# Performance work log

Hardware: AMD Instinct MI355X
Metric: run time of the kernel (lower is better)

Reference implementation:

```python
import jax, jax.numpy as jnp
import numpy as np

B, N, C, H = 8, 1024, 768, 12
D = C // H  # 64


def setup_inputs() -> dict:
    key = jax.random.key(0)
    ks = jax.random.split(key, 6)
    x = jax.random.normal(ks[0], (B, N, C), dtype=jnp.float32)
    pad_mask = jnp.ones((B, N), dtype=jnp.int32)
    # params (torch Linear stored transposed; here kept as (in, out) for x @ W)
    s = 1.0 / np.sqrt(C)
    w_attn = jax.random.uniform(ks[1], (C, 3 * C), jnp.float32, -s, s)
    b_attn = jax.random.uniform(ks[2], (3 * C,), jnp.float32, -s, s)
    w_proj = jax.random.uniform(ks[3], (C, C), jnp.float32, -s, s)
    b_proj = jax.random.uniform(ks[4], (C,), jnp.float32, -s, s)
    return {"x": x, "pad_mask": pad_mask, "w_attn": w_attn,
            "b_attn": b_attn, "w_proj": w_proj, "b_proj": b_proj}


def reference(x, pad_mask, w_attn, b_attn, w_proj, b_proj):
    # qkv projection
    qkv = x @ w_attn + b_attn                      # [B,N,3C]
    q, k, v = jnp.split(qkv, 3, axis=-1)
    q = q.reshape(B, N, H, D).transpose(0, 2, 1, 3)  # [B,H,N,D]
    k = k.reshape(B, N, H, D).transpose(0, 2, 1, 3)
    v = v.reshape(B, N, H, D).transpose(0, 2, 1, 3)
    scale = 1.0 / np.sqrt(D)
    att = jnp.einsum('bhqd,bhkd->bhqk', q, k) * scale  # [B,H,N,N]
    # NOTE: original code's causal masked_fill is non-in-place and discarded,
    # so the causal mask is NOT applied. Only the pad mask (over query rows) is.
    pm = pad_mask.reshape(B, 1, N, 1)
    att = jnp.where(pm == 0, -jnp.inf, att)
    att = jax.nn.softmax(att, axis=-1)
    out = jnp.einsum('bhqk,bhkd->bhqd', att, v)     # [B,H,N,D]
    out = out.transpose(0, 2, 1, 3).reshape(B, N, C)
    # dropout layers are identity in eval mode
    return out @ w_proj + b_proj
```

## Files before the change

### kernel.cpp

```cpp
#include <hip/hip_runtime.h>
#include <hip/hip_bf16.h>

#define B_  8
#define N_  1024
#define C_  768
#define H_  12
#define D_  64
#define C3  2304
#define C2  1536

typedef unsigned short ushort_t;
typedef __attribute__((ext_vector_type(8))) short bf16x8;
typedef __attribute__((ext_vector_type(4))) float f32x4;
typedef __attribute__((ext_vector_type(4))) unsigned int u32x4;
typedef __attribute__((ext_vector_type(2))) unsigned int u32x2;

__device__ __forceinline__ ushort_t f2bf(float f) {
    union { float f; unsigned int i; } v;
    v.f = f;
    unsigned int x = v.i;
    if ((x & 0x7f800000u) == 0x7f800000u && (x & 0x007fffffu))
        return (ushort_t)((x >> 16) | 0x0040u);
    return (ushort_t)((x + 0x7fffu + ((x >> 16) & 1u)) >> 16);
}

__device__ __forceinline__ void st1(float* p, float v) { *p = v; }
__device__ __forceinline__ void st1(ushort_t* p, float v) { *p = f2bf(v); }

__global__ __launch_bounds__(256) void cvt_bf16(
    const float* __restrict__ X, ushort_t* __restrict__ Y, int n)
{
    int i = (blockIdx.x * 256 + threadIdx.x) * 4;
    if (i < n) {
        float4 f = *reinterpret_cast<const float4*>(X + i);
        ushort4 o;
        o.x = f2bf(f.x); o.y = f2bf(f.y); o.z = f2bf(f.z); o.w = f2bf(f.w);
        *reinterpret_cast<ushort4*>(Y + i) = o;
    }
}

__global__ __launch_bounds__(256) void transpose_to_bf16(
    const float* __restrict__ W, ushort_t* __restrict__ WT, int K, int Nn)
{
    __shared__ float t[32][33];
    const int n0 = blockIdx.x * 32, k0 = blockIdx.y * 32;
    const int tx = threadIdx.x & 31, ty = threadIdx.x >> 5;
    #pragma unroll
    for (int i = 0; i < 4; ++i) {
        const int k = ty + i * 8;
        t[k][tx] = W[(size_t)(k0 + k) * Nn + n0 + tx];
    }
    __syncthreads();
    #pragma unroll
    for (int i = 0; i < 4; ++i) {
        const int n = ty + i * 8;
        WT[(size_t)(n0 + n) * K + k0 + tx] = f2bf(t[tx][n]);
    }
}

#define GBK 64

__device__ __forceinline__ void gld_lds16(const ushort_t* g, ushort_t* lds) {
    __builtin_amdgcn_global_load_lds(
        (const __attribute__((address_space(1))) void*)g,
        (__attribute__((address_space(3))) void*)lds, 16, 0, 0);
}

template<typename TO, bool SCALEQ>
__global__ __launch_bounds__(256) void gemm_mfma(
    const ushort_t* __restrict__ A, const ushort_t* __restrict__ BT,
    const float* __restrict__ bias, TO* __restrict__ Y, int ldY,
    ushort_t* __restrict__ vtOut, int M, int K, int Nn)
{
    __shared__ ushort_t As[128 * GBK];
    __shared__ ushort_t Bs[128 * GBK];

    const int tid  = threadIdx.x;
    const int wave = tid >> 6;
    const int lane = tid & 63;
    const int row0 = blockIdx.y * 128;
    const int col0 = blockIdx.x * 128;
    const int wr   = (wave >> 1) * 64;
    const int wc   = (wave & 1) * 64;
    const int l15  = lane & 15;
    const int quad = lane >> 4;
    const int l7   = l15 & 7;

    const int srow = lane >> 3;
    const int sg   = (lane & 7) ^ srow;

    f32x4 acc[4][4] = {};

    for (int k0 = 0; k0 < K; k0 += GBK) {
        __syncthreads();
        #pragma unroll
        for (int it = 0; it < 4; ++it) {
            const int baseRow = wave * 32 + it * 8;
            const int r = baseRow + srow;
            gld_lds16(&A [(size_t)(row0 + r) * K + k0 + sg * 8], &As[baseRow * GBK]);
            gld_lds16(&BT[(size_t)(col0 + r) * K + k0 + sg * 8], &Bs[baseRow * GBK]);
        }
        __syncthreads();

        #pragma unroll
        for (int kc = 0; kc < 2; ++kc) {
            bf16x8 af[4], bf[4];
            #pragma unroll
            for (int i = 0; i < 4; ++i) {
                const int aslot = (kc * 4 + quad) ^ l7;
                af[i] = *reinterpret_cast<const bf16x8*>(
                    &As[(wr + i * 16 + l15) * GBK + aslot * 8]);
                bf[i] = *reinterpret_cast<const bf16x8*>(
                    &Bs[(wc + i * 16 + l15) * GBK + aslot * 8]);
            }
            #pragma unroll
            for (int i = 0; i < 4; ++i)
                #pragma unroll
                for (int j = 0; j < 4; ++j)
                    acc[i][j] = __builtin_amdgcn_mfma_f32_16x16x32_bf16(
                        af[i], bf[j], acc[i][j], 0, 0, 0);
        }
    }

    const float qs = (SCALEQ && (col0 + wc) < C_) ? 0.1803368801f : 1.0f;

    if (vtOut != nullptr && col0 >= C2) {
        #pragma unroll
        for (int i = 0; i < 4; ++i) {
            const int r0 = row0 + wr + i * 16 + quad * 4;
            const int bb = r0 >> 10;
            const int n  = r0 & 1023;
            #pragma unroll
            for (int j = 0; j < 4; ++j) {
                const int c  = col0 + wc + j * 16 + l15;
                const int cv = c - C2;
                const int hh = cv >> 6, d = cv & 63;
                const float bv = bias[c];
                ushort4 o;
                o.x = f2bf(acc[i][j][0] + bv);
                o.y = f2bf(acc[i][j][1] + bv);
                o.z = f2bf(acc[i][j][2] + bv);
                o.w = f2bf(acc[i][j][3] + bv);
                *reinterpret_cast<ushort4*>(
                    &vtOut[((size_t)(bb * H_ + hh) * D_ + d) * N_ + n]) = o;
            }
        }
    } else {
        #pragma unroll
        for (int i = 0; i < 4; ++i) {
            const int r = row0 + wr + i * 16 + quad * 4;
            #pragma unroll
            for (int j = 0; j < 4; ++j) {
                const int c = col0 + wc + j * 16 + l15;
                const float bv = bias[c];
                #pragma unroll
                for (int t = 0; t < 4; ++t)
                    st1(&Y[(size_t)(r + t) * ldY + c], (acc[i][j][t] + bv) * qs);
            }
        }
    }
}

__global__ __launch_bounds__(256) void attn_mfma(
    const ushort_t* __restrict__ qk, const ushort_t* __restrict__ vt,
    const int* __restrict__ pad_mask, ushort_t* __restrict__ y)
{
    __shared__ __align__(16) ushort_t KV[2 * 64 * 64];
    ushort_t* const Ks  = KV;
    ushort_t* const Vts = KV + 64 * 64;

    const int tid  = threadIdx.x;
    const int wave = tid >> 6;
    const int lane = tid & 63;
    const int l15  = lane & 15;
    const int quad = lane >> 4;
    const int l7   = l15 & 7;

    const int qt = blockIdx.x & 7;
    const int h  = (blockIdx.x >> 3) % H_;
    const int b  = blockIdx.x / (8 * H_);
    const int q0 = qt * 128 + wave * 32;

    const ushort_t* qkB = qk + (size_t)b * N_ * C2;
    const ushort_t* vtB = vt + ((size_t)(b * H_ + h)) * D_ * N_;
    const int ho = h * D_;

    bf16x8 qf[2][2];
    #pragma unroll
    for (int rt = 0; rt < 2; ++rt)
        #pragma unroll
        for (int kc = 0; kc < 2; ++kc)
            qf[rt][kc] = *reinterpret_cast<const bf16x8*>(
                &qkB[(size_t)(q0 + rt * 16 + l15) * C2 + ho + kc * 32 + quad * 8]);

    int mrow[2][4];
    #pragma unroll
    for (int rt = 0; rt < 2; ++rt)
        #pragma unroll
        for (int t = 0; t < 4; ++t)
            mrow[rt][t] = pad_mask[b * N_ + q0 + rt * 16 + quad * 4 + t];

    f32x4 oacc[2][4] = {};
    float den[2] = {};

    const int srow = lane >> 3;
    const int sg   = (lane & 7) ^ srow;

    for (int k0 = 0; k0 < N_; k0 += 64) {
        __syncthreads();
        #pragma unroll
        for (int it = 0; it < 2; ++it) {
            const int base = wave * 16 + it * 8;
            const int r = base + srow;
            gld_lds16(&qkB[(size_t)(k0 + r) * C2 + C_ + ho + sg * 8],
                      &Ks[base * 64]);
            gld_lds16(&vtB[(size_t)r * N_ + k0 + sg * 8],
                      &Vts[base * 64]);
        }
        __syncthreads();

        f32x4 s[2][4] = {};
        #pragma unroll
        for (int kc = 0; kc < 2; ++kc) {
            bf16x8 kf[4];
            #pragma unroll
            for (int ct = 0; ct < 4; ++ct) {
                const int slot = (kc * 4 + quad) ^ l7;
                kf[ct] = *reinterpret_cast<const bf16x8*>(
                    &Ks[(ct * 16 + l15) * 64 + slot * 8]);
            }
            __builtin_amdgcn_s_setprio(1);
            #pragma unroll
            for (int rt = 0; rt < 2; ++rt)
                #pragma unroll
                for (int ct = 0; ct < 4; ++ct)
                    s[rt][ct] = __builtin_amdgcn_mfma_f32_16x16x32_bf16(
                        kf[ct], qf[rt][kc], s[rt][ct], 0, 0, 0);
            __builtin_amdgcn_s_setprio(0);
        }

        unsigned pk[2][4][2];
        #pragma unroll
        for (int rt = 0; rt < 2; ++rt)
            #pragma unroll
            for (int ct = 0; ct < 4; ++ct) {
                const unsigned x0 = __float_as_uint(
                    __builtin_amdgcn_exp2f(s[rt][ct][0])) + 0x8000u;
                const unsigned x1 = __float_as_uint(
                    __builtin_amdgcn_exp2f(s[rt][ct][1])) + 0x8000u;
                const unsigned x2 = __float_as_uint(
                    __builtin_amdgcn_exp2f(s[rt][ct][2])) + 0x8000u;
                const unsigned x3 = __float_as_uint(
                    __builtin_amdgcn_exp2f(s[rt][ct][3])) + 0x8000u;
                const unsigned c0 = (x0 >> 16) | (x1 & 0xffff0000u);
                const unsigned c1 = (x2 >> 16) | (x3 & 0xffff0000u);
                den[rt] += __uint_as_float(c0 << 16)
                         + __uint_as_float(c0 & 0xffff0000u)
                         + __uint_as_float(c1 << 16)
                         + __uint_as_float(c1 & 0xffff0000u);
                pk[rt][ct][0] = c0;
                pk[rt][ct][1] = c1;
            }

        #pragma unroll
        for (int kc = 0; kc < 2; ++kc) {
            bf16x8 pf[2], vf[4];
            #pragma unroll
            for (int rt = 0; rt < 2; ++rt) {
                const u32x4 pw = (u32x4){pk[rt][kc * 2][0], pk[rt][kc * 2][1],
                                         pk[rt][kc * 2 + 1][0],
                                         pk[rt][kc * 2 + 1][1]};
                pf[rt] = __builtin_bit_cast(bf16x8, pw);
            }
            #pragma unroll
            for (int dt = 0; dt < 4; ++dt) {
                const int d  = dt * 16 + l15;
                const int g1 = kc * 4 + (quad >> 1);
                const int o  = (quad & 1) * 4;
                const u32x2 va = *reinterpret_cast<const u32x2*>(
                    &Vts[d * 64 + ((g1 ^ l7)) * 8 + o]);
                const u32x2 vb = *reinterpret_cast<const u32x2*>(
                    &Vts[d * 64 + (((g1 + 2) ^ l7)) * 8 + o]);
                const u32x4 wv = __builtin_shufflevector(va, vb, 0, 1, 2, 3);
                vf[dt] = __builtin_bit_cast(bf16x8, wv);
            }
            __builtin_amdgcn_s_setprio(1);
            #pragma unroll
            for (int rt = 0; rt < 2; ++rt)
                #pragma unroll
                for (int dt = 0; dt < 4; ++dt)
                    oacc[rt][dt] = __builtin_amdgcn_mfma_f32_16x16x32_bf16(
                        pf[rt], vf[dt], oacc[rt][dt], 0, 0, 0);
            __builtin_amdgcn_s_setprio(0);
        }
    }

    __syncthreads();
    ushort_t* const scratch = KV + wave * 32 * 64;

    #pragma unroll
    for (int rt = 0; rt < 2; ++rt) {
        float v = den[rt];
        v += __shfl_xor(v, 16);
        v += __shfl_xor(v, 32);
        den[rt] = v;
    }
    #pragma unroll
    for (int rt = 0; rt < 2; ++rt)
        #pragma unroll
        for (int t = 0; t < 4; ++t) {
            const float dv  = __shfl(den[rt], quad * 4 + t);
            const float inv = mrow[rt][t] ? 1.0f / dv : __builtin_nanf("");
            const int row = rt * 16 + quad * 4 + t;
            #pragma unroll
            for (int dt = 0; dt < 4; ++dt) {
                const int slot = (dt * 2 + (l15 >> 3)) ^ (row & 7);
                scratch[row * 64 + slot * 8 + l7] =
                    f2bf(oacc[rt][dt][t] * inv);
            }
        }
    {
        const int orow = lane >> 1;
        const int og   = (lane & 1) * 4;
        const size_t gr = (size_t)(b * N_ + q0 + orow) * C_ + ho;
        #pragma unroll
        for (int i2 = 0; i2 < 4; ++i2) {
            const int g = og + i2;
            uint4 w = *reinterpret_cast<const uint4*>(
                &scratch[orow * 64 + (g ^ (orow & 7)) * 8]);
            *reinterpret_cast<uint4*>(&y[gr + g * 8]) = w;
        }
    }
}

extern "C" void kernel_launch(void* const* d_in, const int* in_sizes, int n_in,
                              void* d_out, int out_size, void* d_ws, size_t ws_size,
                              hipStream_t stream)
{
    const float* x      = (const float*)d_in[0];
    const int*   pad    = (const int*)d_in[1];
    const float* w_attn = (const float*)d_in[2];
    const float* b_attn = (const float*)d_in[3];
    const float* w_proj = (const float*)d_in[4];
    const float* b_proj = (const float*)d_in[5];
    float* out = (float*)d_out;

    ushort_t* qkb = (ushort_t*)d_ws;
    ushort_t* vtb = qkb + (size_t)B_ * N_ * C2;
    ushort_t* y   = vtb + (size_t)B_ * H_ * D_ * N_;
    ushort_t* xb  = y;
    ushort_t* wat = y + (size_t)B_ * N_ * C_;
    ushort_t* wpt = wat + (size_t)C3 * C_;

    const int M = B_ * N_;

    cvt_bf16<<<dim3((M * C_) / (256 * 4)), dim3(256), 0, stream>>>(x, xb, M * C_);
    transpose_to_bf16<<<dim3(C3 / 32, C_ / 32), dim3(256), 0, stream>>>(
        w_attn, wat, C_, C3);
    transpose_to_bf16<<<dim3(C_ / 32, C_ / 32), dim3(256), 0, stream>>>(
        w_proj, wpt, C_, C_);

    gemm_mfma<ushort_t, true><<<dim3(C3 / 128, M / 128), dim3(256), 0, stream>>>(
        xb, wat, b_attn, qkb, C2, vtb, M, C_, C3);

    attn_mfma<<<dim3(B_ * H_ * 8), dim3(256), 0, stream>>>(qkb, vtb, pad, y);

    gemm_mfma<float, false><<<dim3(C_ / 128, M / 128), dim3(256), 0, stream>>>(
        y, wpt, b_proj, out, C_, nullptr, M, C_, C_);
}
```

Measured before the change: 198.9 us.

## Merge prep kernels into one launch and remap block IDs for XCD locality

Folds the x-to-bf16 conversion and the two weight transposes into a single prep kernel, which cuts launch overhead. It also remaps workgroup IDs in the GEMM and attention kernels so that consecutive logical tiles land on the same XCD (hwid&7 striding), aiming for better L2 reuse of shared operands. A __syncthreads is added before the attention epilogue reads scratch, which guards against cross-wave LDS hazards at the cost of one more barrier. The remap assumes the block count is divisible by 8.

```diff
diff --git a/kernel.cpp b/kernel.cpp
--- a/kernel.cpp
+++ b/kernel.cpp
@@ -27,34 +27,50 @@
 __device__ __forceinline__ void st1(float* p, float v) { *p = v; }
 __device__ __forceinline__ void st1(ushort_t* p, float v) { *p = f2bf(v); }
 
-__global__ __launch_bounds__(256) void cvt_bf16(
-    const float* __restrict__ X, ushort_t* __restrict__ Y, int n)
-{
-    int i = (blockIdx.x * 256 + threadIdx.x) * 4;
-    if (i < n) {
+#define NCVT 6144
+#define NTA  1728
+#define NTP  576
+
+__device__ __forceinline__ void transpose_tile(
+    const float* __restrict__ W, ushort_t* __restrict__ WT,
+    int K, int Nn, int n0, int k0, float (*t)[33], int tid)
+{
+    const int tx = tid & 31, ty = tid >> 5;
+    #pragma unroll
+    for (int i = 0; i < 4; ++i) {
+        const int k = ty + i * 8;
+        t[k][tx] = W[(size_t)(k0 + k) * Nn + n0 + tx];
+    }
+    __syncthreads();
+    #pragma unroll
+    for (int i = 0; i < 4; ++i) {
+        const int n = ty + i * 8;
+        WT[(size_t)(n0 + n) * K + k0 + tx] = f2bf(t[tx][n]);
+    }
+}
+
+__global__ __launch_bounds__(256) void prep(
+    const float* __restrict__ X, ushort_t* __restrict__ Y,
+    const float* __restrict__ Wa, ushort_t* __restrict__ WaT,
+    const float* __restrict__ Wp, ushort_t* __restrict__ WpT)
+{
+    __shared__ float t[32][33];
+    const int bid = blockIdx.x;
+    const int tid = threadIdx.x;
+    if (bid < NCVT) {
+        const int i = (bid * 256 + tid) * 4;
         float4 f = *reinterpret_cast<const float4*>(X + i);
         ushort4 o;
         o.x = f2bf(f.x); o.y = f2bf(f.y); o.z = f2bf(f.z); o.w = f2bf(f.w);
         *reinterpret_cast<ushort4*>(Y + i) = o;
-    }
-}
-
-__global__ __launch_bounds__(256) void transpose_to_bf16(
-    const float* __restrict__ W, ushort_t* __restrict__ WT, int K, int Nn)
-{
-    __shared__ float t[32][33];
-    const int n0 = blockIdx.x * 32, k0 = blockIdx.y * 32;
-    const int tx = threadIdx.x & 31, ty = threadIdx.x >> 5;
-    #pragma unroll
-    for (int i = 0; i < 4; ++i) {
-        const int k = ty + i * 8;
-        t[k][tx] = W[(size_t)(k0 + k) * Nn + n0 + tx];
-    }
-    __syncthreads();
-    #pragma unroll
-    for (int i = 0; i < 4; ++i) {
-        const int n = ty + i * 8;
-        WT[(size_t)(n0 + n) * K + k0 + tx] = f2bf(t[tx][n]);
+    } else if (bid < NCVT + NTA) {
+        const int tt = bid - NCVT;
+        transpose_tile(Wa, WaT, C_, C3, (tt % (C3 / 32)) * 32,
+                       (tt / (C3 / 32)) * 32, t, tid);
+    } else {
+        const int tt = bid - NCVT - NTA;
+        transpose_tile(Wp, WpT, C_, C_, (tt % (C_ / 32)) * 32,
+                       (tt / (C_ / 32)) * 32, t, tid);
     }
 }
 
@@ -78,8 +94,14 @@
     const int tid  = threadIdx.x;
     const int wave = tid >> 6;
     const int lane = tid & 63;
-    const int row0 = blockIdx.y * 128;
-    const int col0 = blockIdx.x * 128;
+
+    const int nbx  = Nn / 128;
+    const int nblk = nbx * (M / 128);
+    const int hwid = blockIdx.y * gridDim.x + blockIdx.x;
+    const int wid  = (hwid & 7) * (nblk >> 3) + (hwid >> 3);
+    const int row0 = (wid / nbx) * 128;
+    const int col0 = (wid % nbx) * 128;
+
     const int wr   = (wave >> 1) * 64;
     const int wc   = (wave & 1) * 64;
     const int l15  = lane & 15;
@@ -176,9 +198,11 @@
     const int quad = lane >> 4;
     const int l7   = l15 & 7;
 
-    const int qt = blockIdx.x & 7;
-    const int h  = (blockIdx.x >> 3) % H_;
-    const int b  = blockIdx.x / (8 * H_);
+    const int wid = (blockIdx.x & 7) * 96 + (blockIdx.x >> 3);
+    const int qt = wid & 7;
+    const int hb = wid >> 3;
+    const int h  = hb % H_;
+    const int b  = hb / H_;
     const int q0 = qt * 128 + wave * 32;
 
     const ushort_t* qkB = qk + (size_t)b * N_ * C2;
@@ -319,6 +343,7 @@
                     f2bf(oacc[rt][dt][t] * inv);
             }
         }
+    __syncthreads();
     {
         const int orow = lane >> 1;
         const int og   = (lane & 1) * 4;
@@ -354,11 +379,8 @@
 
     const int M = B_ * N_;
 
-    cvt_bf16<<<dim3((M * C_) / (256 * 4)), dim3(256), 0, stream>>>(x, xb, M * C_);
-    transpose_to_bf16<<<dim3(C3 / 32, C_ / 32), dim3(256), 0, stream>>>(
-        w_attn, wat, C_, C3);
-    transpose_to_bf16<<<dim3(C_ / 32, C_ / 32), dim3(256), 0, stream>>>(
-        w_proj, wpt, C_, C_);
+    prep<<<dim3(NCVT + NTA + NTP), dim3(256), 0, stream>>>(
+        x, xb, w_attn, wat, w_proj, wpt);
 
     gemm_mfma<ushort_t, true><<<dim3(C3 / 128, M / 128), dim3(256), 0, stream>>>(
         xb, wat, b_attn, qkb, C2, vtb, M, C_, C3);
```

Result: faster. 192.9 us (-3.0%).
